# Kernel optimization log

Measured on AMD Instinct MI355X. Metric: run time of the kernel, lower is better.

## Reference

```python
import jax, jax.numpy as jnp
import numpy as np


def setup_inputs() -> dict:
    key = jax.random.key(0)
    x = jax.random.normal(key, (128, 256, 32, 32), dtype=jnp.float32)
    return {"x": x, "iter_num": 5}


def reference(x, iter_num):
    # x: (B, C, H, W)
    B, C, H, W = x.shape
    N = H * W
    xr = x.reshape(B, C, N)
    # Covariance pooling: X @ I_hat @ X^T == (1/N) * Xc @ Xc^T  (I_hat = I/N - J/N^2)
    xc = xr - xr.mean(axis=2, keepdims=True)
    cov = jnp.einsum('bcn,bdn->bcd', xc, xc) / N  # (B, C, C)

    # Newton-Schulz iterative matrix square root
    I = jnp.eye(C, dtype=x.dtype)
    I3 = 3.0 * I
    trace = jnp.trace(cov, axis1=1, axis2=2)[:, None, None]  # norm_A = tr(cov)
    A = cov / trace
    ZY = 0.5 * (I3 - A)
    Y = A @ ZY
    Z = ZY
    for _ in range(1, iter_num - 1):
        ZY = 0.5 * (I3 - Z @ Y)
        Y = Y @ ZY
        Z = ZY @ Z
    YZY = 0.5 * (Y @ (I3 - Z @ Y))
    sqrtm = YZY * jnp.sqrt(trace)  # (B, C, C)

    # Upper-triangular vectorization (row-major, including diagonal)
    r, c = np.triu_indices(C)
    idx = jnp.asarray(r * C + c)
    return sqrtm.reshape(B, C * C)[:, idx]  # (B, C*(C+1)//2)
```

## Files before the change

### kernel.cpp

```cpp
#include <hip/hip_runtime.h>
#include <hip/hip_fp16.h>


typedef _Float16 half8 __attribute__((ext_vector_type(8)));
typedef _Float16 half4 __attribute__((ext_vector_type(4)));
typedef float f32x4 __attribute__((ext_vector_type(4)));

#define OUTPB 32896

__device__ __forceinline__ void gl_lds16(const void* g, void* l) {
  __builtin_amdgcn_global_load_lds(
      (const __attribute__((address_space(1))) void*)g,
      (__attribute__((address_space(3))) void*)l, 16, 0, 0);
}

#define VMB(N) asm volatile("s_waitcnt vmcnt(" #N ")\n\ts_barrier" ::: "memory")
#define LKB()  asm volatile("s_waitcnt lgkmcnt(0)\n\ts_barrier" ::: "memory")

__device__ __forceinline__ void tile_pq(int t, int& p, int& q) {
  p = (t > 3) + (t > 6) + (t > 8);
  int base = p * 4 - (p * (p - 1)) / 2;
  q = p + (t - base);
}

__device__ __forceinline__ half8 cvt8(float4 a, float4 b) {
  half8 h;
  h[0] = (_Float16)a.x; h[1] = (_Float16)a.y; h[2] = (_Float16)a.z; h[3] = (_Float16)a.w;
  h[4] = (_Float16)b.x; h[5] = (_Float16)b.y; h[6] = (_Float16)b.z; h[7] = (_Float16)b.w;
  return h;
}

__device__ __forceinline__ void mfma64(const _Float16* lA, const _Float16* lB,
                                       f32x4 (&acc)[2][2], int wr, int wc,
                                       int lr, int lk) {
#pragma unroll
  for (int ks = 0; ks < 2; ++ks) {
    half8 af[2], bf[2];
#pragma unroll
    for (int m = 0; m < 2; ++m) {
      int row = wr * 32 + m * 16 + lr;
      int kc = (ks * 4 + lk) ^ (row & 7);
      af[m] = *(const half8*)&lA[row * 64 + kc * 8];
    }
#pragma unroll
    for (int n = 0; n < 2; ++n) {
      int row = wc * 32 + n * 16 + lr;
      int kc = (ks * 4 + lk) ^ (row & 7);
      bf[n] = *(const half8*)&lB[row * 64 + kc * 8];
    }
    __builtin_amdgcn_s_setprio(1);
#pragma unroll
    for (int m = 0; m < 2; ++m)
#pragma unroll
      for (int n = 0; n < 2; ++n)
        acc[m][n] = __builtin_amdgcn_mfma_f32_16x16x32_f16(af[m], bf[n], acc[m][n], 0, 0, 0);
    __builtin_amdgcn_s_setprio(0);
  }
}

__device__ __forceinline__ void gemm64(const _Float16* Ap, const _Float16* Bp,
    bool share, _Float16* lds, f32x4 (&acc)[2][2], int tid) {
  const int w = tid >> 6, lane = tid & 63;
  auto stageH = [&](const _Float16* panel, int buf, int base, int kk) {
#pragma unroll
    for (int i = 0; i < 2; ++i) {
      int s = (w * 2 + i) * 64 + lane;
      int row = s >> 3, cst = s & 7;
      int kc = cst ^ (row & 7);
      gl_lds16(panel + (size_t)row * 256 + kk * 64 + kc * 8,
               &lds[base + buf * 4096 + (w * 2 + i) * 512]);
    }
  };
  const int wr = w >> 1, wc = w & 1, lr = lane & 15, lk = lane >> 4;
  stageH(Ap, 0, 0, 0);
  if (!share) stageH(Bp, 0, 8192, 0);
#pragma unroll 1
  for (int kk = 0; kk < 4; ++kk) {
    int cur = kk & 1;
    if (kk < 3) {
      stageH(Ap, cur ^ 1, 0, kk + 1);
      if (!share) {
        stageH(Bp, cur ^ 1, 8192, kk + 1);
        VMB(4);
      } else {
        VMB(2);
      }
    } else {
      VMB(0);
    }
    mfma64(&lds[cur * 4096], share ? &lds[cur * 4096] : &lds[8192 + cur * 4096],
           acc, wr, wc, lr, lk);
    LKB();
  }
}

__global__ __launch_bounds__(256, 2) void k_cov(const float* __restrict__ x,
                                                _Float16* __restrict__ covh,
                                                float* __restrict__ trPart) {
  __shared__ _Float16 lds[32768];
  __shared__ float sred[4];

  const int lin = blockIdx.x + 3 * blockIdx.y;
  const int cid = (lin & 7) * 48 + (lin >> 3);
  const int b = cid / 3, t = cid - 3 * b;
  const int p = (t == 1), q = (t != 0);
  const bool diag = (t < 2);
  const int tid = threadIdx.x, w = tid >> 6, lane = tid & 63;
  const int wr = w >> 1, wc = w & 1, lr = lane & 15, lk = lane >> 4;

  const float* Ab = x + ((size_t)b * 256 + p * 128) * 1024;
  const float* Bb = x + ((size_t)b * 256 + q * 128) * 1024;

  float4 la[4][2], lb[4][2];
  f32x4 acc[4][4] = {};
  f32x4 rsA[4] = {}, rsB[4] = {};
  half8 ones;
#pragma unroll
  for (int i = 0; i < 8; ++i) ones[i] = (_Float16)1.0f;

  auto LOAD = [&](int kk) {
#pragma unroll
    for (int i = 0; i < 4; ++i) {
      int u = i * 256 + tid;
      int row = u >> 3, c8 = u & 7;
      int kc = c8 ^ (row & 7);
      const float* sa = Ab + (size_t)row * 1024 + kk * 64 + kc * 8;
      la[i][0] = *(const float4*)sa; la[i][1] = *(const float4*)(sa + 4);
      if (!diag) {
        const float* sb = Bb + (size_t)row * 1024 + kk * 64 + kc * 8;
        lb[i][0] = *(const float4*)sb; lb[i][1] = *(const float4*)(sb + 4);
      }
    }
  };
  auto WRITE = [&](int buf) {
#pragma unroll
    for (int i = 0; i < 4; ++i) {
      int u = i * 256 + tid;
      *(half8*)&lds[buf * 8192 + u * 8] = cvt8(la[i][0], la[i][1]);
      if (!diag) *(half8*)&lds[16384 + buf * 8192 + u * 8] = cvt8(lb[i][0], lb[i][1]);
    }
  };
  auto STEP = [&](const _Float16* lA, const _Float16* lB) {
#pragma unroll
    for (int ks = 0; ks < 2; ++ks) {
      half8 af[4], bf[4];
#pragma unroll
      for (int m = 0; m < 4; ++m) {
        int row = wr * 64 + m * 16 + lr;
        int kc = (ks * 4 + lk) ^ (row & 7);
        af[m] = *(const half8*)&lA[row * 64 + kc * 8];
      }
#pragma unroll
      for (int n = 0; n < 4; ++n) {
        int row = wc * 64 + n * 16 + lr;
        int kc = (ks * 4 + lk) ^ (row & 7);
        bf[n] = *(const half8*)&lB[row * 64 + kc * 8];
      }
      __builtin_amdgcn_s_setprio(1);
#pragma unroll
      for (int m = 0; m < 4; ++m)
        rsA[m] = __builtin_amdgcn_mfma_f32_16x16x32_f16(af[m], ones, rsA[m], 0, 0, 0);
#pragma unroll
      for (int n = 0; n < 4; ++n)
        rsB[n] = __builtin_amdgcn_mfma_f32_16x16x32_f16(ones, bf[n], rsB[n], 0, 0, 0);
#pragma unroll
      for (int m = 0; m < 4; ++m)
#pragma unroll
        for (int n = 0; n < 4; ++n)
          acc[m][n] = __builtin_amdgcn_mfma_f32_16x16x32_f16(af[m], bf[n], acc[m][n], 0, 0, 0);
      __builtin_amdgcn_s_setprio(0);
    }
  };

  LOAD(0); WRITE(0); LOAD(1);
  __syncthreads();
#pragma unroll 1
  for (int kk = 0; kk < 16; ++kk) {
    int cur = kk & 1;
    STEP(&lds[cur * 8192], diag ? &lds[cur * 8192] : &lds[16384 + cur * 8192]);
    if (kk < 15) {
      WRITE(cur ^ 1);
      if (kk < 14) LOAD(kk + 2);
    }
    __syncthreads();
  }

  const float inv = 1.f / 1024.f;
  if (diag) {
    float tp = 0.f;
#pragma unroll
    for (int m = 0; m < 4; ++m)
#pragma unroll
      for (int n = 0; n < 4; ++n)
#pragma unroll
        for (int r = 0; r < 4; ++r) {
          int il = wr * 64 + m * 16 + lk * 4 + r, jl = wc * 64 + n * 16 + lr;
          if (il == jl) tp += (acc[m][n][r] - rsA[m][r] * rsB[n][0] * inv) * inv;
        }
#pragma unroll
    for (int o = 32; o; o >>= 1) tp += __shfl_down(tp, o);
    if (lane == 0) sred[w] = tp;
    __syncthreads();
    if (tid == 0) trPart[b * 2 + p] = sred[0] + sred[1] + sred[2] + sred[3];
  }

  const size_t boff = (size_t)b * 65536;
#pragma unroll
  for (int m = 0; m < 4; ++m)
#pragma unroll
    for (int n = 0; n < 4; ++n) {
      int il0 = wr * 64 + m * 16 + lk * 4;
      int jl = wc * 64 + n * 16 + lr;
      half4 v4;
#pragma unroll
      for (int r = 0; r < 4; ++r) {
        int il = il0 + r;
        float cv = (acc[m][n][r] - rsA[m][r] * rsB[n][0] * inv) * inv;
        v4[r] = (_Float16)cv;
        if (!diag) lds[il * 128 + (((jl >> 3) ^ (il & 7)) << 3) + (jl & 7)] = v4[r];
      }
      *(half4*)&covh[boff + (size_t)(q * 128 + jl) * 256 + p * 128 + il0] = v4;
    }
  if (!diag) {
    __syncthreads();
#pragma unroll
    for (int pp = 0; pp < 8; ++pp) {
      int u = pp * 256 + tid;
      int im = u >> 4, cu = u & 15;
      half8 v8 = *(const half8*)&lds[im * 128 + ((cu ^ (im & 7)) << 3)];
      *(half8*)&covh[boff + (size_t)(p * 128 + im) * 256 + q * 128 + cu * 8] = v8;
    }
  }
}

__global__ __launch_bounds__(256, 4) void k_s2(const _Float16* __restrict__ covh,
                                               const float* __restrict__ trP,
                                               _Float16* __restrict__ Y0,
                                               _Float16* __restrict__ Z0) {
  __shared__ _Float16 lds[16384];
  const int lin = blockIdx.x + 10 * blockIdx.y;
  const int cid = (lin & 7) * 160 + (lin >> 3);
  const int b = cid / 10, t = cid - 10 * b;
  int p, q; tile_pq(t, p, q);
  const bool diag = (p == q);
  const int tid = threadIdx.x, w = tid >> 6, lane = tid & 63;
  const int wr = w >> 1, wc = w & 1, lr = lane & 15, lk = lane >> 4;
  const size_t boff = (size_t)b * 65536;

  f32x4 acc[2][2] = {};
  gemm64(covh + boff + (size_t)p * 64 * 256, covh + boff + (size_t)q * 64 * 256,
         diag, lds, acc, tid);

  float tv = trP[b * 2] + trP[b * 2 + 1];
  float it1 = 1.f / tv;
  _Float16* TY = lds;
  _Float16* TZ = lds + 4096;
#pragma unroll
  for (int m = 0; m < 2; ++m)
#pragma unroll
    for (int n = 0; n < 2; ++n) {
      int il0 = wr * 32 + m * 16 + lk * 4;
      int jl = wc * 32 + n * 16 + lr;
      half4 c4 = *(const half4*)&covh[boff + (size_t)(q * 64 + jl) * 256 + p * 64 + il0];
      half4 y4, z4;
#pragma unroll
      for (int r = 0; r < 4; ++r) {
        int i = p * 64 + il0 + r, j = q * 64 + jl;
        float c = (float)c4[r];
        y4[r] = (_Float16)(1.5f * c * it1 - 0.5f * acc[m][n][r] * it1 * it1);
        z4[r] = (_Float16)((i == j ? 1.5f : 0.f) - 0.5f * c * it1);
        if (!diag) {
          int sp = (il0 + r) * 64 + (jl ^ (((il0 + r) & 7) << 3));
          TY[sp] = y4[r]; TZ[sp] = z4[r];
        }
      }
      *(half4*)&Y0[boff + (size_t)(q * 64 + jl) * 256 + p * 64 + il0] = y4;
      *(half4*)&Z0[boff + (size_t)(q * 64 + jl) * 256 + p * 64 + il0] = z4;
    }
  if (!diag) {
    __syncthreads();
#pragma unroll
    for (int pp = 0; pp < 2; ++pp) {
      int u = pp * 256 + tid;
      int im = u >> 3, cu = u & 7;
      half8 vy = *(const half8*)&TY[im * 64 + ((cu ^ (im & 7)) << 3)];
      half8 vz = *(const half8*)&TZ[im * 64 + ((cu ^ (im & 7)) << 3)];
      *(half8*)&Y0[boff + (size_t)(p * 64 + im) * 256 + q * 64 + cu * 8] = vy;
      *(half8*)&Z0[boff + (size_t)(p * 64 + im) * 256 + q * 64 + cu * 8] = vz;
    }
  }
}


#define IT_STAGE_RES(SRC)                                                  \
  {                                                                        \
    _Pragma("unroll") for (int i = 0; i < 8; ++i) {                        \
      int s = i * 256 + tid;                                               \
      int row = s >> 5, cp = s & 31;                                       \
      int c = cp ^ (row & 7);                                              \
      gl_lds16((SRC) + (size_t)(q * 64 + row) * 256 + c * 8, &lds[s * 8]); \
    }                                                                      \
  }

struct ITP {
  const _Float16 *Y, *Z;
  _Float16 *Yn, *Zn;
  const float* trP;
  float* outF;
};

template <bool FINAL>
__global__ __launch_bounds__(256, 2) void k_it(ITP P) {
  __shared__ _Float16 lds[32768];
  const int lin = blockIdx.x + 4 * blockIdx.y;
  const int cid = (lin & 7) * 64 + (lin >> 3);
  const int b = cid >> 2, q = cid & 3;
  const int tid = threadIdx.x, w = tid >> 6, lane = tid & 63;
  const int lr = lane & 15, lk = lane >> 4;
  const size_t boff = (size_t)b * 65536;
  const _Float16* Yg = P.Y + boff;
  const _Float16* Zg = P.Z + boff;

  auto stage = [&](const _Float16* M, int buf, int kk) {
#pragma unroll
    for (int i = 0; i < 4; ++i) {
      int s = i * 256 + tid;
      int row = s >> 2, cp = s & 3;
      int c = cp ^ (row & 3);
      gl_lds16(M + (size_t)row * 256 + kk * 32 + c * 8,
               &lds[16384 + buf * 8192 + s * 8]);
    }
  };

  f32x4 acc[4][4];
  auto zero = [&]() {
#pragma unroll
    for (int m = 0; m < 4; ++m)
#pragma unroll
      for (int n = 0; n < 4; ++n) {
        f32x4 z = {0.f, 0.f, 0.f, 0.f};
        acc[m][n] = z;
      }
  };

  auto stepRA = [&](int kk, int cur) {
    half8 af[4], bf[4];
    const _Float16* sb = &lds[16384 + cur * 8192];
#pragma unroll
    for (int m = 0; m < 4; ++m) {
      int row = m * 16 + lr;
      int c = (kk * 4 + lk) ^ (row & 7);
      af[m] = *(const half8*)&lds[row * 256 + c * 8];
    }
#pragma unroll
    for (int n = 0; n < 4; ++n) {
      int row = w * 64 + n * 16 + lr;
      int cp = lk ^ (row & 3);
      bf[n] = *(const half8*)&sb[row * 32 + cp * 8];
    }
    __builtin_amdgcn_s_setprio(1);
#pragma unroll
    for (int m = 0; m < 4; ++m)
#pragma unroll
      for (int n = 0; n < 4; ++n)
        acc[m][n] = __builtin_amdgcn_mfma_f32_16x16x32_f16(af[m], bf[n], acc[m][n], 0, 0, 0);
    __builtin_amdgcn_s_setprio(0);
  };
  auto stepRB = [&](int kk, int cur) {
    half8 af[4], bf[4];
    const _Float16* sa = &lds[16384 + cur * 8192];
#pragma unroll
    for (int m = 0; m < 4; ++m) {
      int row = w * 64 + m * 16 + lr;
      int cp = lk ^ (row & 3);
      af[m] = *(const half8*)&sa[row * 32 + cp * 8];
    }
#pragma unroll
    for (int n = 0; n < 4; ++n) {
      int row = n * 16 + lr;
      int c = (kk * 4 + lk) ^ (row & 7);
      bf[n] = *(const half8*)&lds[row * 256 + c * 8];
    }
    __builtin_amdgcn_s_setprio(1);
#pragma unroll
    for (int m = 0; m < 4; ++m)
#pragma unroll
      for (int n = 0; n < 4; ++n)
        acc[m][n] = __builtin_amdgcn_mfma_f32_16x16x32_f16(af[m], bf[n], acc[m][n], 0, 0, 0);
    __builtin_amdgcn_s_setprio(0);
  };

  zero();
  IT_STAGE_RES(Zg);
  stage(Yg, 0, 0);
#pragma unroll 1
  for (int kk = 0; kk < 8; ++kk) {
    int cur = kk & 1;
    if (kk < 7) { stage(Yg, cur ^ 1, kk + 1); VMB(4); } else { VMB(0); }
    stepRA(kk, cur);
    LKB();
  }
#pragma unroll
  for (int m = 0; m < 4; ++m)
#pragma unroll
    for (int n = 0; n < 4; ++n) {
      int kcol = w * 64 + n * 16 + lr;
#pragma unroll
      for (int r = 0; r < 4; ++r) {
        int j = m * 16 + lk * 4 + r;
        float v = (kcol == q * 64 + j ? 1.5f : 0.f) - 0.5f * acc[m][n][r];
        lds[j * 256 + (((kcol >> 3) ^ (j & 7)) << 3) + (kcol & 7)] = (_Float16)v;
      }
    }
  __syncthreads();

  zero();
  stage(Yg, 0, 0);
#pragma unroll 1
  for (int kk = 0; kk < 8; ++kk) {
    int cur = kk & 1;
    if (kk < 7) { stage(Yg, cur ^ 1, kk + 1); VMB(4); } else { VMB(0); }
    stepRB(kk, cur);
    LKB();
  }

  if constexpr (!FINAL) {
#pragma unroll
    for (int m = 0; m < 4; ++m)
#pragma unroll
      for (int n = 0; n < 4; ++n) {
        int jg = q * 64 + n * 16 + lr;
        int i0 = w * 64 + m * 16 + lk * 4;
        half4 v4;
#pragma unroll
        for (int r = 0; r < 4; ++r) v4[r] = (_Float16)acc[m][n][r];
        *(half4*)&P.Yn[boff + (size_t)jg * 256 + i0] = v4;
      }

    zero();
    stage(Zg, 0, 0);
#pragma unroll 1
    for (int kk = 0; kk < 8; ++kk) {
      int cur = kk & 1;
      if (kk < 7) { stage(Zg, cur ^ 1, kk + 1); VMB(4); } else { VMB(0); }
      stepRB(kk, cur);
      LKB();
    }
#pragma unroll
    for (int m = 0; m < 4; ++m)
#pragma unroll
      for (int n = 0; n < 4; ++n) {
        int jg = q * 64 + n * 16 + lr;
        int i0 = w * 64 + m * 16 + lk * 4;
        half4 v4;
#pragma unroll
        for (int r = 0; r < 4; ++r) v4[r] = (_Float16)acc[m][n][r];
        *(half4*)&P.Zn[boff + (size_t)jg * 256 + i0] = v4;
      }
  } else {
    float tv = P.trP[b * 2] + P.trP[b * 2 + 1];
    float st = sqrtf(tv);
#pragma unroll
    for (int m = 0; m < 4; ++m)
#pragma unroll
      for (int n = 0; n < 4; ++n) {
        int jg = q * 64 + n * 16 + lr;
        int i0 = w * 64 + m * 16 + lk * 4;
#pragma unroll
        for (int r = 0; r < 4; ++r) {
          int i = i0 + r;
          if (i <= jg) {
            int idx = jg + i * 256 - (i * (i + 1)) / 2;
            P.outF[(size_t)b * OUTPB + idx] = acc[m][n][r] * st;
          }
        }
      }
  }
}

extern "C" void kernel_launch(void* const* d_in, const int* in_sizes, int n_in,
                              void* d_out, int out_size, void* d_ws, size_t ws_size,
                              hipStream_t stream) {
  const float* x = (const float*)d_in[0];
  float* outF = (float*)d_out;

  char* ws = (char*)d_ws;
  const size_t MATB = (size_t)128 * 65536 * sizeof(_Float16);
  _Float16* covh = (_Float16*)ws;
  _Float16* Y0   = (_Float16*)(ws + MATB);
  _Float16* Z0   = (_Float16*)(ws + 2 * MATB);
  _Float16* Y1   = (_Float16*)(ws + 3 * MATB);
  _Float16* Z1   = (_Float16*)(ws + 4 * MATB);
  float* trP     = (float*)(ws + 5 * MATB);

  dim3 g3(3, 128), g10(10, 128), g4(4, 128);

  k_cov<<<g3, 256, 0, stream>>>(x, covh, trP);
  k_s2<<<g10, 256, 0, stream>>>(covh, trP, Y0, Z0);

  _Float16 *Yc = Y0, *Zc = Z0, *Yn = Y1, *Zn = Z1;
  for (int itn = 0; itn < 3; ++itn) {
    ITP p{};
    p.Y = Yc; p.Z = Zc; p.Yn = Yn; p.Zn = Zn;
    k_it<false><<<g4, 256, 0, stream>>>(p);
    _Float16* t0 = Yc; Yc = Yn; Yn = t0;
    _Float16* t1 = Zc; Zc = Zn; Zn = t1;
  }
  {
    ITP p{};
    p.Y = Yc; p.Z = Zc; p.trP = trP; p.outF = outF;
    k_it<true><<<g4, 256, 0, stream>>>(p);
  }
}
```

Baseline: 158.5 us.

## Rebalance covariance tiling, replace first NS step kernel, triple-buffer iteration loads

The covariance kernel now splits each batch into four work items: two diagonal 128x128 blocks and two 128x64 off-diagonal blocks. This balances work across a 4-wide grid instead of three uneven tiles. The separate first-step kernel, which computed A@A via 10 small tiles, is replaced by k_first. k_first builds Z from the resident covariance strip and computes Y as cov@Z scaled by 1/trace, reusing the column-strip iteration structure. The iteration kernels move from double to triple buffering of global-to-LDS staging with fully unrolled k-loops, which raises LDS use per block to hide load latency. The cost is lower occupancy headroom.

```diff
diff --git a/kernel.cpp b/kernel.cpp
--- a/kernel.cpp
+++ b/kernel.cpp
@@ -16,12 +16,6 @@
 
 #define VMB(N) asm volatile("s_waitcnt vmcnt(" #N ")\n\ts_barrier" ::: "memory")
 #define LKB()  asm volatile("s_waitcnt lgkmcnt(0)\n\ts_barrier" ::: "memory")
-
-__device__ __forceinline__ void tile_pq(int t, int& p, int& q) {
-  p = (t > 3) + (t > 6) + (t > 8);
-  int base = p * 4 - (p * (p - 1)) / 2;
-  q = p + (t - base);
-}
 
 __device__ __forceinline__ half8 cvt8(float4 a, float4 b) {
   half8 h;
@@ -30,88 +24,25 @@
   return h;
 }
 
-__device__ __forceinline__ void mfma64(const _Float16* lA, const _Float16* lB,
-                                       f32x4 (&acc)[2][2], int wr, int wc,
-                                       int lr, int lk) {
-#pragma unroll
-  for (int ks = 0; ks < 2; ++ks) {
-    half8 af[2], bf[2];
-#pragma unroll
-    for (int m = 0; m < 2; ++m) {
-      int row = wr * 32 + m * 16 + lr;
-      int kc = (ks * 4 + lk) ^ (row & 7);
-      af[m] = *(const half8*)&lA[row * 64 + kc * 8];
-    }
-#pragma unroll
-    for (int n = 0; n < 2; ++n) {
-      int row = wc * 32 + n * 16 + lr;
-      int kc = (ks * 4 + lk) ^ (row & 7);
-      bf[n] = *(const half8*)&lB[row * 64 + kc * 8];
-    }
-    __builtin_amdgcn_s_setprio(1);
-#pragma unroll
-    for (int m = 0; m < 2; ++m)
-#pragma unroll
-      for (int n = 0; n < 2; ++n)
-        acc[m][n] = __builtin_amdgcn_mfma_f32_16x16x32_f16(af[m], bf[n], acc[m][n], 0, 0, 0);
-    __builtin_amdgcn_s_setprio(0);
-  }
-}
-
-__device__ __forceinline__ void gemm64(const _Float16* Ap, const _Float16* Bp,
-    bool share, _Float16* lds, f32x4 (&acc)[2][2], int tid) {
-  const int w = tid >> 6, lane = tid & 63;
-  auto stageH = [&](const _Float16* panel, int buf, int base, int kk) {
-#pragma unroll
-    for (int i = 0; i < 2; ++i) {
-      int s = (w * 2 + i) * 64 + lane;
-      int row = s >> 3, cst = s & 7;
-      int kc = cst ^ (row & 7);
-      gl_lds16(panel + (size_t)row * 256 + kk * 64 + kc * 8,
-               &lds[base + buf * 4096 + (w * 2 + i) * 512]);
-    }
-  };
-  const int wr = w >> 1, wc = w & 1, lr = lane & 15, lk = lane >> 4;
-  stageH(Ap, 0, 0, 0);
-  if (!share) stageH(Bp, 0, 8192, 0);
-#pragma unroll 1
-  for (int kk = 0; kk < 4; ++kk) {
-    int cur = kk & 1;
-    if (kk < 3) {
-      stageH(Ap, cur ^ 1, 0, kk + 1);
-      if (!share) {
-        stageH(Bp, cur ^ 1, 8192, kk + 1);
-        VMB(4);
-      } else {
-        VMB(2);
-      }
-    } else {
-      VMB(0);
-    }
-    mfma64(&lds[cur * 4096], share ? &lds[cur * 4096] : &lds[8192 + cur * 4096],
-           acc, wr, wc, lr, lk);
-    LKB();
-  }
-}
-
 __global__ __launch_bounds__(256, 2) void k_cov(const float* __restrict__ x,
                                                 _Float16* __restrict__ covh,
                                                 float* __restrict__ trPart) {
-  __shared__ _Float16 lds[32768];
+  __shared__ _Float16 lds[24576];
   __shared__ float sred[4];
 
-  const int lin = blockIdx.x + 3 * blockIdx.y;
-  const int cid = (lin & 7) * 48 + (lin >> 3);
-  const int b = cid / 3, t = cid - 3 * b;
-  const int p = (t == 1), q = (t != 0);
+  const int lin = blockIdx.x + 4 * blockIdx.y;
+  const int cid = (lin & 7) * 64 + (lin >> 3);
+  const int b = cid >> 2, t = cid & 3;
   const bool diag = (t < 2);
+  const int p = diag ? t : 0;
+  const int uoff = diag ? 0 : (t - 2);
   const int tid = threadIdx.x, w = tid >> 6, lane = tid & 63;
   const int wr = w >> 1, wc = w & 1, lr = lane & 15, lk = lane >> 4;
 
   const float* Ab = x + ((size_t)b * 256 + p * 128) * 1024;
-  const float* Bb = x + ((size_t)b * 256 + q * 128) * 1024;
-
-  float4 la[4][2], lb[4][2];
+  const float* Bb = x + ((size_t)b * 256 + 128 + 64 * uoff) * 1024;
+
+  float4 la[4][2], lb[2][2];
   f32x4 acc[4][4] = {};
   f32x4 rsA[4] = {}, rsB[4] = {};
   half8 ones;
@@ -121,12 +52,18 @@
   auto LOAD = [&](int kk) {
 #pragma unroll
     for (int i = 0; i < 4; ++i) {
-      int u = i * 256 + tid;
-      int row = u >> 3, c8 = u & 7;
+      int u2 = i * 256 + tid;
+      int row = u2 >> 3, c8 = u2 & 7;
       int kc = c8 ^ (row & 7);
       const float* sa = Ab + (size_t)row * 1024 + kk * 64 + kc * 8;
       la[i][0] = *(const float4*)sa; la[i][1] = *(const float4*)(sa + 4);
-      if (!diag) {
+    }
+    if (!diag) {
+#pragma unroll
+      for (int i = 0; i < 2; ++i) {
+        int u2 = i * 256 + tid;
+        int row = u2 >> 3, c8 = u2 & 7;
+        int kc = c8 ^ (row & 7);
         const float* sb = Bb + (size_t)row * 1024 + kk * 64 + kc * 8;
         lb[i][0] = *(const float4*)sb; lb[i][1] = *(const float4*)(sb + 4);
       }
@@ -135,12 +72,20 @@
   auto WRITE = [&](int buf) {
 #pragma unroll
     for (int i = 0; i < 4; ++i) {
-      int u = i * 256 + tid;
-      *(half8*)&lds[buf * 8192 + u * 8] = cvt8(la[i][0], la[i][1]);
-      if (!diag) *(half8*)&lds[16384 + buf * 8192 + u * 8] = cvt8(lb[i][0], lb[i][1]);
-    }
-  };
-  auto STEP = [&](const _Float16* lA, const _Float16* lB) {
+      int u2 = i * 256 + tid;
+      *(half8*)&lds[buf * 8192 + u2 * 8] = cvt8(la[i][0], la[i][1]);
+    }
+    if (!diag) {
+#pragma unroll
+      for (int i = 0; i < 2; ++i) {
+        int u2 = i * 256 + tid;
+        *(half8*)&lds[16384 + buf * 4096 + u2 * 8] = cvt8(lb[i][0], lb[i][1]);
+      }
+    }
+  };
+  auto STEP = [&](int cur) {
+    const _Float16* lA = &lds[cur * 8192];
+    const _Float16* lB = &lds[16384 + cur * 4096];
 #pragma unroll
     for (int ks = 0; ks < 2; ++ks) {
       half8 af[4], bf[4];
@@ -150,24 +95,44 @@
         int kc = (ks * 4 + lk) ^ (row & 7);
         af[m] = *(const half8*)&lA[row * 64 + kc * 8];
       }
-#pragma unroll
-      for (int n = 0; n < 4; ++n) {
-        int row = wc * 64 + n * 16 + lr;
-        int kc = (ks * 4 + lk) ^ (row & 7);
-        bf[n] = *(const half8*)&lB[row * 64 + kc * 8];
+      if (diag) {
+#pragma unroll
+        for (int n = 0; n < 4; ++n) {
+          int row = wc * 64 + n * 16 + lr;
+          int kc = (ks * 4 + lk) ^ (row & 7);
+          bf[n] = *(const half8*)&lA[row * 64 + kc * 8];
+        }
+      } else {
+#pragma unroll
+        for (int n = 0; n < 2; ++n) {
+          int jloc = wc * 32 + n * 16 + lr;
+          int kc = (ks * 4 + lk) ^ (jloc & 7);
+          bf[n] = *(const half8*)&lB[jloc * 64 + kc * 8];
+        }
       }
       __builtin_amdgcn_s_setprio(1);
 #pragma unroll
       for (int m = 0; m < 4; ++m)
         rsA[m] = __builtin_amdgcn_mfma_f32_16x16x32_f16(af[m], ones, rsA[m], 0, 0, 0);
-#pragma unroll
-      for (int n = 0; n < 4; ++n)
-        rsB[n] = __builtin_amdgcn_mfma_f32_16x16x32_f16(ones, bf[n], rsB[n], 0, 0, 0);
-#pragma unroll
-      for (int m = 0; m < 4; ++m)
+      if (diag) {
 #pragma unroll
         for (int n = 0; n < 4; ++n)
-          acc[m][n] = __builtin_amdgcn_mfma_f32_16x16x32_f16(af[m], bf[n], acc[m][n], 0, 0, 0);
+          rsB[n] = __builtin_amdgcn_mfma_f32_16x16x32_f16(ones, bf[n], rsB[n], 0, 0, 0);
+#pragma unroll
+        for (int m = 0; m < 4; ++m)
+#pragma unroll
+          for (int n = 0; n < 4; ++n)
+            acc[m][n] = __builtin_amdgcn_mfma_f32_16x16x32_f16(af[m], bf[n], acc[m][n], 0, 0, 0);
+      } else {
+#pragma unroll
+        for (int n = 0; n < 2; ++n)
+          rsB[n] = __builtin_amdgcn_mfma_f32_16x16x32_f16(ones, bf[n], rsB[n], 0, 0, 0);
+#pragma unroll
+        for (int m = 0; m < 4; ++m)
+#pragma unroll
+          for (int n = 0; n < 2; ++n)
+            acc[m][n] = __builtin_amdgcn_mfma_f32_16x16x32_f16(af[m], bf[n], acc[m][n], 0, 0, 0);
+      }
       __builtin_amdgcn_s_setprio(0);
     }
   };
@@ -177,7 +142,7 @@
 #pragma unroll 1
   for (int kk = 0; kk < 16; ++kk) {
     int cur = kk & 1;
-    STEP(&lds[cur * 8192], diag ? &lds[cur * 8192] : &lds[16384 + cur * 8192]);
+    STEP(cur);
     if (kk < 15) {
       WRITE(cur ^ 1);
       if (kk < 14) LOAD(kk + 2);
@@ -186,6 +151,8 @@
   }
 
   const float inv = 1.f / 1024.f;
+  const size_t boff = (size_t)b * 65536;
+
   if (diag) {
     float tp = 0.f;
 #pragma unroll
@@ -202,91 +169,44 @@
     if (lane == 0) sred[w] = tp;
     __syncthreads();
     if (tid == 0) trPart[b * 2 + p] = sred[0] + sred[1] + sred[2] + sred[3];
-  }
-
-  const size_t boff = (size_t)b * 65536;
-#pragma unroll
-  for (int m = 0; m < 4; ++m)
-#pragma unroll
-    for (int n = 0; n < 4; ++n) {
-      int il0 = wr * 64 + m * 16 + lk * 4;
-      int jl = wc * 64 + n * 16 + lr;
-      half4 v4;
-#pragma unroll
-      for (int r = 0; r < 4; ++r) {
-        int il = il0 + r;
-        float cv = (acc[m][n][r] - rsA[m][r] * rsB[n][0] * inv) * inv;
-        v4[r] = (_Float16)cv;
-        if (!diag) lds[il * 128 + (((jl >> 3) ^ (il & 7)) << 3) + (jl & 7)] = v4[r];
-      }
-      *(half4*)&covh[boff + (size_t)(q * 128 + jl) * 256 + p * 128 + il0] = v4;
-    }
-  if (!diag) {
+
+#pragma unroll
+    for (int m = 0; m < 4; ++m)
+#pragma unroll
+      for (int n = 0; n < 4; ++n) {
+        int il0 = wr * 64 + m * 16 + lk * 4;
+        int jl = wc * 64 + n * 16 + lr;
+        half4 v4;
+#pragma unroll
+        for (int r = 0; r < 4; ++r)
+          v4[r] = (_Float16)((acc[m][n][r] - rsA[m][r] * rsB[n][0] * inv) * inv);
+        *(half4*)&covh[boff + (size_t)(p * 128 + jl) * 256 + p * 128 + il0] = v4;
+      }
+  } else {
+#pragma unroll
+    for (int m = 0; m < 4; ++m)
+#pragma unroll
+      for (int n = 0; n < 2; ++n) {
+        int il0 = wr * 64 + m * 16 + lk * 4;
+        int jl = wc * 32 + n * 16 + lr;
+        int jg = 128 + 64 * uoff + jl;
+        half4 v4;
+#pragma unroll
+        for (int r = 0; r < 4; ++r) {
+          int il = il0 + r;
+          float cv = (acc[m][n][r] - rsA[m][r] * rsB[n][0] * inv) * inv;
+          v4[r] = (_Float16)cv;
+          lds[il * 64 + (((jl >> 3) ^ (il & 7)) << 3) + (jl & 7)] = v4[r];
+        }
+        *(half4*)&covh[boff + (size_t)jg * 256 + il0] = v4;
+      }
     __syncthreads();
 #pragma unroll
-    for (int pp = 0; pp < 8; ++pp) {
-      int u = pp * 256 + tid;
-      int im = u >> 4, cu = u & 15;
-      half8 v8 = *(const half8*)&lds[im * 128 + ((cu ^ (im & 7)) << 3)];
-      *(half8*)&covh[boff + (size_t)(p * 128 + im) * 256 + q * 128 + cu * 8] = v8;
-    }
-  }
-}
-
-__global__ __launch_bounds__(256, 4) void k_s2(const _Float16* __restrict__ covh,
-                                               const float* __restrict__ trP,
-                                               _Float16* __restrict__ Y0,
-                                               _Float16* __restrict__ Z0) {
-  __shared__ _Float16 lds[16384];
-  const int lin = blockIdx.x + 10 * blockIdx.y;
-  const int cid = (lin & 7) * 160 + (lin >> 3);
-  const int b = cid / 10, t = cid - 10 * b;
-  int p, q; tile_pq(t, p, q);
-  const bool diag = (p == q);
-  const int tid = threadIdx.x, w = tid >> 6, lane = tid & 63;
-  const int wr = w >> 1, wc = w & 1, lr = lane & 15, lk = lane >> 4;
-  const size_t boff = (size_t)b * 65536;
-
-  f32x4 acc[2][2] = {};
-  gemm64(covh + boff + (size_t)p * 64 * 256, covh + boff + (size_t)q * 64 * 256,
-         diag, lds, acc, tid);
-
-  float tv = trP[b * 2] + trP[b * 2 + 1];
-  float it1 = 1.f / tv;
-  _Float16* TY = lds;
-  _Float16* TZ = lds + 4096;
-#pragma unroll
-  for (int m = 0; m < 2; ++m)
-#pragma unroll
-    for (int n = 0; n < 2; ++n) {
-      int il0 = wr * 32 + m * 16 + lk * 4;
-      int jl = wc * 32 + n * 16 + lr;
-      half4 c4 = *(const half4*)&covh[boff + (size_t)(q * 64 + jl) * 256 + p * 64 + il0];
-      half4 y4, z4;
-#pragma unroll
-      for (int r = 0; r < 4; ++r) {
-        int i = p * 64 + il0 + r, j = q * 64 + jl;
-        float c = (float)c4[r];
-        y4[r] = (_Float16)(1.5f * c * it1 - 0.5f * acc[m][n][r] * it1 * it1);
-        z4[r] = (_Float16)((i == j ? 1.5f : 0.f) - 0.5f * c * it1);
-        if (!diag) {
-          int sp = (il0 + r) * 64 + (jl ^ (((il0 + r) & 7) << 3));
-          TY[sp] = y4[r]; TZ[sp] = z4[r];
-        }
-      }
-      *(half4*)&Y0[boff + (size_t)(q * 64 + jl) * 256 + p * 64 + il0] = y4;
-      *(half4*)&Z0[boff + (size_t)(q * 64 + jl) * 256 + p * 64 + il0] = z4;
-    }
-  if (!diag) {
-    __syncthreads();
-#pragma unroll
-    for (int pp = 0; pp < 2; ++pp) {
-      int u = pp * 256 + tid;
-      int im = u >> 3, cu = u & 7;
-      half8 vy = *(const half8*)&TY[im * 64 + ((cu ^ (im & 7)) << 3)];
-      half8 vz = *(const half8*)&TZ[im * 64 + ((cu ^ (im & 7)) << 3)];
-      *(half8*)&Y0[boff + (size_t)(p * 64 + im) * 256 + q * 64 + cu * 8] = vy;
-      *(half8*)&Z0[boff + (size_t)(p * 64 + im) * 256 + q * 64 + cu * 8] = vz;
+    for (int pp = 0; pp < 4; ++pp) {
+      int v = pp * 256 + tid;
+      int im = v >> 3, cu = v & 7;
+      half8 v8 = *(const half8*)&lds[im * 64 + ((cu ^ (im & 7)) << 3)];
+      *(half8*)&covh[boff + (size_t)im * 256 + 128 + 64 * uoff + cu * 8] = v8;
     }
   }
 }
@@ -302,6 +222,130 @@
     }                                                                      \
   }
 
+#define IT_IDS                                                   \
+  const int lin = blockIdx.x + 4 * blockIdx.y;                   \
+  const int cid = (lin & 7) * 64 + (lin >> 3);                   \
+  const int b = cid >> 2, q = cid & 3;                           \
+  const int tid = threadIdx.x, w = tid >> 6, lane = tid & 63;    \
+  const int lr = lane & 15, lk = lane >> 4;                      \
+  const size_t boff = (size_t)b * 65536;
+
+#define IT_ZERO                                                  \
+  _Pragma("unroll") for (int m = 0; m < 4; ++m)                  \
+  _Pragma("unroll") for (int n = 0; n < 4; ++n) {                \
+    f32x4 z = {0.f, 0.f, 0.f, 0.f};                              \
+    acc[m][n] = z;                                               \
+  }
+
+#define IT3_LOOP(M, STEPFN)                                   \
+  stage(M, 0, 0); stage(M, 1, 1);                             \
+  _Pragma("unroll") for (int kk = 0; kk < 8; ++kk) {          \
+    int cur = kk % 3;                                         \
+    if (kk < 6) { stage(M, (kk + 2) % 3, kk + 2); VMB(8); }   \
+    else if (kk == 6) { VMB(4); }                             \
+    else { VMB(0); }                                          \
+    STEPFN(kk, cur);                                          \
+    LKB();                                                    \
+  }
+
+#define DEF_STAGE                                              \
+  auto stage = [&](const _Float16* M, int buf, int kk) {       \
+    _Pragma("unroll") for (int i = 0; i < 4; ++i) {            \
+      int s = i * 256 + tid;                                   \
+      int row = s >> 2, cp = s & 3;                            \
+      int c = cp ^ (row & 3);                                  \
+      gl_lds16(M + (size_t)row * 256 + kk * 32 + c * 8,        \
+               &lds[16384 + buf * 8192 + s * 8]);              \
+    }                                                          \
+  };
+
+#define DEF_STEPRB                                                         \
+  auto stepRB = [&](int kk, int cur) {                                     \
+    half8 af[4], bf[4];                                                    \
+    const _Float16* sa = &lds[16384 + cur * 8192];                         \
+    _Pragma("unroll") for (int m = 0; m < 4; ++m) {                        \
+      int row = w * 64 + m * 16 + lr;                                      \
+      int cp = lk ^ (row & 3);                                             \
+      af[m] = *(const half8*)&sa[row * 32 + cp * 8];                       \
+    }                                                                      \
+    _Pragma("unroll") for (int n = 0; n < 4; ++n) {                        \
+      int row = n * 16 + lr;                                               \
+      int c = (kk * 4 + lk) ^ (row & 7);                                   \
+      bf[n] = *(const half8*)&lds[row * 256 + c * 8];                      \
+    }                                                                      \
+    __builtin_amdgcn_s_setprio(1);                                         \
+    _Pragma("unroll") for (int m = 0; m < 4; ++m)                          \
+    _Pragma("unroll") for (int n = 0; n < 4; ++n)                          \
+      acc[m][n] = __builtin_amdgcn_mfma_f32_16x16x32_f16(af[m], bf[n], acc[m][n], 0, 0, 0); \
+    __builtin_amdgcn_s_setprio(0);                                         \
+  };
+
+#define IT_STORE(DST)                                                   \
+  _Pragma("unroll") for (int m = 0; m < 4; ++m)                         \
+  _Pragma("unroll") for (int n = 0; n < 4; ++n) {                       \
+    int jg = q * 64 + n * 16 + lr;                                      \
+    int i0 = w * 64 + m * 16 + lk * 4;                                  \
+    half4 v4;                                                           \
+    _Pragma("unroll") for (int r = 0; r < 4; ++r) v4[r] = (_Float16)acc[m][n][r]; \
+    *(half4*)&(DST)[boff + (size_t)jg * 256 + i0] = v4;                 \
+  }
+
+__global__ __launch_bounds__(256, 2) void k_first(const _Float16* __restrict__ covh,
+                                                  const float* __restrict__ trP,
+                                                  _Float16* __restrict__ Y1,
+                                                  _Float16* __restrict__ Z1) {
+  __shared__ _Float16 lds[40960];
+  IT_IDS;
+  const _Float16* Cg = covh + boff;
+  const float tv = trP[b * 2] + trP[b * 2 + 1];
+  const float it1 = 1.f / tv;
+
+  IT_STAGE_RES(Cg);
+  VMB(0);
+#pragma unroll
+  for (int i = 0; i < 8; ++i) {
+    int s = i * 256 + tid;
+    int row = s >> 5, cp = s & 31;
+    int c = cp ^ (row & 7);
+    half8 v = *(const half8*)&lds[s * 8];
+    half8 wv;
+#pragma unroll
+    for (int e = 0; e < 8; ++e) {
+      int col = c * 8 + e;
+      float f = -0.5f * it1 * (float)v[e] + ((col == q * 64 + row) ? 1.5f : 0.f);
+      wv[e] = (_Float16)f;
+    }
+    *(half8*)&lds[s * 8] = wv;
+  }
+  __syncthreads();
+
+  DEF_STAGE;
+  f32x4 acc[4][4];
+  DEF_STEPRB;
+
+  IT_ZERO;
+  IT3_LOOP(Cg, stepRB);
+
+#pragma unroll
+  for (int m = 0; m < 4; ++m)
+#pragma unroll
+    for (int n = 0; n < 4; ++n) {
+      int jg = q * 64 + n * 16 + lr;
+      int i0 = w * 64 + m * 16 + lk * 4;
+      half4 v4;
+#pragma unroll
+      for (int r = 0; r < 4; ++r) v4[r] = (_Float16)(acc[m][n][r] * it1);
+      *(half4*)&Y1[boff + (size_t)jg * 256 + i0] = v4;
+    }
+#pragma unroll
+  for (int i = 0; i < 8; ++i) {
+    int s = i * 256 + tid;
+    int row = s >> 5, cL = s & 31;
+    half8 v = *(const half8*)&lds[(row * 32 + (cL ^ (row & 7))) * 8];
+    *(half8*)&Z1[boff + (size_t)(q * 64 + row) * 256 + cL * 8] = v;
+  }
+}
+
 struct ITP {
   const _Float16 *Y, *Z;
   _Float16 *Yn, *Zn;
@@ -310,38 +354,15 @@
 };
 
 template <bool FINAL>
-__global__ __launch_bounds__(256, 2) void k_it(ITP P) {
-  __shared__ _Float16 lds[32768];
-  const int lin = blockIdx.x + 4 * blockIdx.y;
-  const int cid = (lin & 7) * 64 + (lin >> 3);
-  const int b = cid >> 2, q = cid & 3;
-  const int tid = threadIdx.x, w = tid >> 6, lane = tid & 63;
-  const int lr = lane & 15, lk = lane >> 4;
-  const size_t boff = (size_t)b * 65536;
+__global__ __launch_bounds__(256, 2) void k_it3(ITP P) {
+  __shared__ _Float16 lds[40960];
+  IT_IDS;
   const _Float16* Yg = P.Y + boff;
   const _Float16* Zg = P.Z + boff;
 
-  auto stage = [&](const _Float16* M, int buf, int kk) {
-#pragma unroll
-    for (int i = 0; i < 4; ++i) {
-      int s = i * 256 + tid;
-      int row = s >> 2, cp = s & 3;
-      int c = cp ^ (row & 3);
-      gl_lds16(M + (size_t)row * 256 + kk * 32 + c * 8,
-               &lds[16384 + buf * 8192 + s * 8]);
-    }
-  };
-
+  DEF_STAGE;
   f32x4 acc[4][4];
-  auto zero = [&]() {
-#pragma unroll
-    for (int m = 0; m < 4; ++m)
-#pragma unroll
-      for (int n = 0; n < 4; ++n) {
-        f32x4 z = {0.f, 0.f, 0.f, 0.f};
-        acc[m][n] = z;
-      }
-  };
+  DEF_STEPRB;
 
   auto stepRA = [&](int kk, int cur) {
     half8 af[4], bf[4];
@@ -366,40 +387,10 @@
         acc[m][n] = __builtin_amdgcn_mfma_f32_16x16x32_f16(af[m], bf[n], acc[m][n], 0, 0, 0);
     __builtin_amdgcn_s_setprio(0);
   };
-  auto stepRB = [&](int kk, int cur) {
-    half8 af[4], bf[4];
-    const _Float16* sa = &lds[16384 + cur * 8192];
-#pragma unroll
-    for (int m = 0; m < 4; ++m) {
-      int row = w * 64 + m * 16 + lr;
-      int cp = lk ^ (row & 3);
-      af[m] = *(const half8*)&sa[row * 32 + cp * 8];
-    }
-#pragma unroll
-    for (int n = 0; n < 4; ++n) {
-      int row = n * 16 + lr;
-      int c = (kk * 4 + lk) ^ (row & 7);
-      bf[n] = *(const half8*)&lds[row * 256 + c * 8];
-    }
-    __builtin_amdgcn_s_setprio(1);
-#pragma unroll
-    for (int m = 0; m < 4; ++m)
-#pragma unroll
-      for (int n = 0; n < 4; ++n)
-        acc[m][n] = __builtin_amdgcn_mfma_f32_16x16x32_f16(af[m], bf[n], acc[m][n], 0, 0, 0);
-    __builtin_amdgcn_s_setprio(0);
-  };
-
-  zero();
+
+  IT_ZERO;
   IT_STAGE_RES(Zg);
-  stage(Yg, 0, 0);
-#pragma unroll 1
-  for (int kk = 0; kk < 8; ++kk) {
-    int cur = kk & 1;
-    if (kk < 7) { stage(Yg, cur ^ 1, kk + 1); VMB(4); } else { VMB(0); }
-    stepRA(kk, cur);
-    LKB();
-  }
+  IT3_LOOP(Yg, stepRA);
 #pragma unroll
   for (int m = 0; m < 4; ++m)
 #pragma unroll
@@ -414,49 +405,14 @@
     }
   __syncthreads();
 
-  zero();
-  stage(Yg, 0, 0);
-#pragma unroll 1
-  for (int kk = 0; kk < 8; ++kk) {
-    int cur = kk & 1;
-    if (kk < 7) { stage(Yg, cur ^ 1, kk + 1); VMB(4); } else { VMB(0); }
-    stepRB(kk, cur);
-    LKB();
-  }
+  IT_ZERO;
+  IT3_LOOP(Yg, stepRB);
 
   if constexpr (!FINAL) {
-#pragma unroll
-    for (int m = 0; m < 4; ++m)
-#pragma unroll
-      for (int n = 0; n < 4; ++n) {
-        int jg = q * 64 + n * 16 + lr;
-        int i0 = w * 64 + m * 16 + lk * 4;
-        half4 v4;
-#pragma unroll
-        for (int r = 0; r < 4; ++r) v4[r] = (_Float16)acc[m][n][r];
-        *(half4*)&P.Yn[boff + (size_t)jg * 256 + i0] = v4;
-      }
-
-    zero();
-    stage(Zg, 0, 0);
-#pragma unroll 1
-    for (int kk = 0; kk < 8; ++kk) {
-      int cur = kk & 1;
-      if (kk < 7) { stage(Zg, cur ^ 1, kk + 1); VMB(4); } else { VMB(0); }
-      stepRB(kk, cur);
-      LKB();
-    }
-#pragma unroll
-    for (int m = 0; m < 4; ++m)
-#pragma unroll
-      for (int n = 0; n < 4; ++n) {
-        int jg = q * 64 + n * 16 + lr;
-        int i0 = w * 64 + m * 16 + lk * 4;
-        half4 v4;
-#pragma unroll
-        for (int r = 0; r < 4; ++r) v4[r] = (_Float16)acc[m][n][r];
-        *(half4*)&P.Zn[boff + (size_t)jg * 256 + i0] = v4;
-      }
+    IT_STORE(P.Yn);
+    IT_ZERO;
+    IT3_LOOP(Zg, stepRB);
+    IT_STORE(P.Zn);
   } else {
     float tv = P.trP[b * 2] + P.trP[b * 2 + 1];
     float st = sqrtf(tv);
@@ -493,22 +449,22 @@
   _Float16* Z1   = (_Float16*)(ws + 4 * MATB);
   float* trP     = (float*)(ws + 5 * MATB);
 
-  dim3 g3(3, 128), g10(10, 128), g4(4, 128);
-
-  k_cov<<<g3, 256, 0, stream>>>(x, covh, trP);
-  k_s2<<<g10, 256, 0, stream>>>(covh, trP, Y0, Z0);
+  dim3 g4(4, 128);
+
+  k_cov<<<g4, 256, 0, stream>>>(x, covh, trP);
+  k_first<<<g4, 256, 0, stream>>>(covh, trP, Y0, Z0);
 
   _Float16 *Yc = Y0, *Zc = Z0, *Yn = Y1, *Zn = Z1;
   for (int itn = 0; itn < 3; ++itn) {
     ITP p{};
     p.Y = Yc; p.Z = Zc; p.Yn = Yn; p.Zn = Zn;
-    k_it<false><<<g4, 256, 0, stream>>>(p);
+    k_it3<false><<<g4, 256, 0, stream>>>(p);
     _Float16* t0 = Yc; Yc = Yn; Yn = t0;
     _Float16* t1 = Zc; Zc = Zn; Zn = t1;
   }
   {
     ITP p{};
     p.Y = Yc; p.Z = Zc; p.trP = trP; p.outF = outF;
-    k_it<true><<<g4, 256, 0, stream>>>(p);
-  }
-}
+    k_it3<true><<<g4, 256, 0, stream>>>(p);
+  }
+}
```

Measured after the change: 150.4 us. 5.1% less time.
